# Kernel optimization log

Hardware: AMD Instinct MI355X
Metric: run time of the kernel (lower is better)

Reference implementation:

```python
import jax, jax.numpy as jnp
import numpy as np

MAX_Z = 54  # atomic numbers up to iodine (53)
_mv = np.full(MAX_Z, 4.0, np.float32)
for z, v in {6: 4, 7: 3, 8: 2, 16: 6, 9: 1, 17: 1, 35: 1, 53: 1, 15: 5, 1: 1}.items():
    _mv[z] = v
_vdw = np.full(MAX_Z, 1.6, np.float32)  # default_radius = 1.6
for z, r in {1: 1.2, 6: 1.7, 7: 1.55, 8: 1.52, 9: 1.47, 15: 1.8, 16: 1.8, 17: 1.75, 35: 1.85, 53: 1.98}.items():
    _vdw[z] = r
_bl = np.full((MAX_Z, MAX_Z), 1.5, np.float32)  # default_length = 1.5
for (a, b), L in {(6, 6): 1.54, (6, 7): 1.47, (6, 8): 1.43, (6, 16): 1.82, (6, 9): 1.35, (6, 17): 1.77, (6, 1): 1.09, (7, 7): 1.45, (7, 8): 1.40, (7, 1): 1.01, (8, 8): 1.48, (8, 1): 0.96, (16, 16): 2.05, (15, 8): 1.63}.items():
    _bl[a, b] = L
    _bl[b, a] = L  # symmetric == tuple(sorted(...)) lookup
MAX_VAL = jnp.asarray(_mv)
VDW = jnp.asarray(_vdw)
BOND = jnp.asarray(_bl)
BIG = 1e9  # stands in for torch's float('inf') diagonal mask


def _forward(pos, edge_index, atom_types):
    N = pos.shape[0]
    row, col = edge_index[0], edge_index[1]
    # --- valence violations: scatter-add out-degree per atom ---
    bond_counts = jnp.zeros((N,), pos.dtype).at[row].add(1.0)
    violation = jnp.maximum(bond_counts - MAX_VAL[atom_types], 0.0)  # >0 iff counts > max_val
    loss = jnp.sum(violation ** 2)
    # Sequential valence push. Original loops atoms in ascending order and each atom's
    # neighbors in edge-list order; a stable sort of edges by row reproduces exactly that
    # visitation order, so a scan over sorted edges matches the sequential semantics
    # (pos_new[i] updates feed later direction computations).
    order = jnp.argsort(row)  # jnp.argsort is stable
    rs, cs = row[order], col[order]

    def step(p, rc):
        r, c = rc
        v = violation[r]
        d = p[r] - p[c]
        dist = jnp.linalg.norm(d) + 1e-8
        return p.at[r].add(jnp.where(v > 0, d / dist * v * 1e-3, 0.0)), None

    pos_new, _ = jax.lax.scan(step, pos, (rs, cs))
    # --- bond-length correction (gather per edge, scatter back per atom) ---
    bond_vec = pos_new[row] - pos_new[col]                        # [E,3]
    cur_len = jnp.linalg.norm(bond_vec, axis=-1, keepdims=True)   # [E,1]
    tgt_len = BOND[atom_types[row], atom_types[col]][:, None]     # [E,1]
    loss = loss + jnp.mean(jnp.abs(cur_len - tgt_len) ** 2)
    ratio = jnp.clip(tgt_len / (cur_len + 1e-8), 0.98, 1.02)
    adj = (bond_vec * ratio - bond_vec) * 0.01
    pos_new = pos_new + jnp.zeros_like(pos).at[row].add(adj * 0.5).at[col].add(-adj * 0.5)
    # --- steric clash repulsion over all atom pairs (cdist) ---
    sq = jnp.sum(pos_new ** 2, axis=-1)
    d2 = sq[:, None] + sq[None, :] - 2.0 * (pos_new @ pos_new.T)  # [N,N]
    eye = jnp.eye(N, dtype=bool)
    dist = jnp.sqrt(jnp.maximum(jnp.where(eye, 1.0, d2), 1e-20))
    dist = jnp.where(eye, BIG, dist)  # diagonal masked to +inf in the original
    rad = VDW[atom_types]
    min_d = (rad[:, None] + rad[None, :]) * 0.8
    loss = loss + jnp.sum(jax.nn.relu(min_d - dist) ** 2) / 2.0
    # original loops unordered clash pairs i<j updating i and j symmetrically; the full
    # symmetric double sum below is mathematically identical and avoids an [N,N,3] tensor:
    mask = (dist < min_d) & (dist > 1e-8)
    coeff = jnp.where(mask, (min_d - dist) * 0.005 * 0.5 / dist, 0.0)  # [N,N]
    steric = coeff.sum(axis=1)[:, None] * pos_new - coeff @ pos_new    # sum_j c_ij (p_i - p_j)
    return pos_new + steric, loss * 0.1


def setup_inputs() -> dict:
    key = jax.random.key(0)
    k1, k2, k3, k4 = jax.random.split(key, 4)
    N, E = 8192, 32768
    pos = jax.random.normal(k1, (N, 3), jnp.float32) * 6.0  # coords in an ~Angstrom-scale blob
    elements = jnp.array([1, 6, 7, 8, 9, 15, 16, 17], jnp.int32)  # H C N O F P S Cl
    atom_types = elements[jax.random.randint(k2, (N,), 0, 8)]
    edge_index = jnp.stack([jax.random.randint(k3, (E,), 0, N),
                            jax.random.randint(k4, (E,), 0, N)]).astype(jnp.int32)
    return {"pos": pos, "edge_index": edge_index, "atom_types": atom_types}


def reference(pos, edge_index, atom_types):
    return _forward(pos, edge_index, atom_types)
```

## Files before the change

### kernel.cpp

```cpp
#include <hip/hip_runtime.h>
#include <math.h>

#define NA 8192
#define NE 32768
#define NT 256

#define WS_DEG      0
#define WS_LOSS     (WS_DEG + NA)
#define WS_DD       (WS_LOSS + 4)
#define WS_ZERO_END (WS_DD + 3*NA)
#define WS_PART     ((WS_ZERO_END + 3) & ~3)

__device__ __forceinline__ float maxval_of(int z) {
    switch (z) {
        case 1: return 1.f; case 6: return 4.f; case 7: return 3.f; case 8: return 2.f;
        case 9: return 1.f; case 15: return 5.f; case 16: return 6.f; case 17: return 1.f;
        case 35: return 1.f; case 53: return 1.f; default: return 4.f;
    }
}
__device__ __forceinline__ float vdw_of(int z) {
    switch (z) {
        case 1: return 1.2f; case 6: return 1.7f; case 7: return 1.55f; case 8: return 1.52f;
        case 9: return 1.47f; case 15: return 1.8f; case 16: return 1.8f; case 17: return 1.75f;
        case 35: return 1.85f; case 53: return 1.98f; default: return 1.6f;
    }
}
__device__ __forceinline__ float bond_of(int a, int b) {
    int lo = a < b ? a : b, hi = a < b ? b : a;
    switch (lo * 64 + hi) {
        case 6*64+6:   return 1.54f;
        case 6*64+7:   return 1.47f;
        case 6*64+8:   return 1.43f;
        case 6*64+16:  return 1.82f;
        case 6*64+9:   return 1.35f;
        case 6*64+17:  return 1.77f;
        case 1*64+6:   return 1.09f;
        case 7*64+7:   return 1.45f;
        case 7*64+8:   return 1.40f;
        case 1*64+7:   return 1.01f;
        case 8*64+8:   return 1.48f;
        case 1*64+8:   return 0.96f;
        case 16*64+16: return 2.05f;
        case 8*64+15:  return 1.63f;
        default:       return 1.5f;
    }
}
__device__ __forceinline__ float viol_of(int d, int z) {
    return fmaxf((float)d - maxval_of(z), 0.f);
}

__device__ __forceinline__ float wave_reduce_sum(float x) {
    #pragma unroll
    for (int off = 32; off > 0; off >>= 1) x += __shfl_down(x, off);
    return x;
}

__global__ void k_deg(const int* __restrict__ row, int* __restrict__ deg) {
    int e = blockIdx.x * NT + threadIdx.x;
    if (e < NE) atomicAdd(&deg[row[e]], 1);
}

__global__ void k_edge(const int* __restrict__ row, const int* __restrict__ col,
                       const int* __restrict__ types, const int* __restrict__ deg,
                       const float* __restrict__ pos, float* __restrict__ dD,
                       float* __restrict__ lossAcc) {
    int e = blockIdx.x * NT + threadIdx.x;
    float l1 = 0.f, l0 = 0.f;
    if (e < NE) {
        int r = row[e], c = col[e];
        float bx = pos[3*r]   - pos[3*c];
        float by = pos[3*r+1] - pos[3*c+1];
        float bz = pos[3*r+2] - pos[3*c+2];
        float cur = sqrtf(bx*bx + by*by + bz*bz);
        float tgt = bond_of(types[r], types[c]);
        float diff = cur - tgt;
        l1 = diff * diff;
        float ratio = tgt / (cur + 1e-8f);
        ratio = fminf(fmaxf(ratio, 0.98f), 1.02f);
        float s = (ratio - 1.f) * 0.01f * 0.5f;
        float v = viol_of(deg[r], types[r]);
        float sc = (v > 0.f) ? (v * 1e-3f / (cur + 1e-8f)) : 0.f;
        float rs = s + sc;
        atomicAdd(&dD[3*r],   bx * rs);
        atomicAdd(&dD[3*r+1], by * rs);
        atomicAdd(&dD[3*r+2], bz * rs);
        atomicAdd(&dD[3*c],   -bx * s);
        atomicAdd(&dD[3*c+1], -by * s);
        atomicAdd(&dD[3*c+2], -bz * s);
    }
    if (e < NA) {
        float v = viol_of(deg[e], types[e]);
        l0 = v * v;
    }
    float p1 = wave_reduce_sum(l1);
    float p0 = wave_reduce_sum(l0);
    if ((threadIdx.x & 63) == 0) {
        if (p1 != 0.f) atomicAdd(&lossAcc[1], p1);
        if (p0 != 0.f) atomicAdd(&lossAcc[0], p0);
    }
}

__device__ __forceinline__ void steric_pair(const float4 p, const float4 q,
                                            float& sx, float& sy, float& sz,
                                            float& ll) {
    float dx = p.x - q.x, dy = p.y - q.y, dz = p.z - q.z;
    float d2 = fmaf(dx, dx, fmaf(dy, dy, dz * dz));
    float md = p.w + q.w;
    float rinv = rsqrtf(fmaxf(d2, 1e-12f));
    float dist = d2 * rinv;
    float t1 = fmaxf(md - dist, 0.f);
    float t1c = (d2 > 1e-12f) ? t1 : 0.f;
    ll = fmaf(t1c, t1c, ll);
    float co = t1c * rinv;
    sx = fmaf(co, dx, sx);
    sy = fmaf(co, dy, sy);
    sz = fmaf(co, dz, sz);
}

template<int JSPLIT>
__global__ void __launch_bounds__(NT)
k_steric(const float* __restrict__ pos, const float* __restrict__ dD,
         const int* __restrict__ types, float4* __restrict__ partial,
         float* __restrict__ lossAcc) {
    constexpr int JCHUNK = NA / JSPLIT;
    constexpr int NIB    = NA / (NT * 2);
    __shared__ float4 sm[JCHUNK];
    const int t = threadIdx.x;
    const int b = blockIdx.x;
    const int yb = b / NIB;
    const int ib = b % NIB;
    if (t < JCHUNK) {
        int j = yb * JCHUNK + t;
        sm[t] = make_float4(pos[3*j]   + dD[3*j],
                            pos[3*j+1] + dD[3*j+1],
                            pos[3*j+2] + dD[3*j+2],
                            vdw_of(types[j]) * 0.8f);
    }
    const int i0 = ib * (NT * 2) + t;
    const int i1 = i0 + NT;
    float4 p0 = make_float4(pos[3*i0] + dD[3*i0], pos[3*i0+1] + dD[3*i0+1],
                            pos[3*i0+2] + dD[3*i0+2], vdw_of(types[i0]) * 0.8f);
    float4 p1 = make_float4(pos[3*i1] + dD[3*i1], pos[3*i1+1] + dD[3*i1+1],
                            pos[3*i1+2] + dD[3*i1+2], vdw_of(types[i1]) * 0.8f);
    __syncthreads();
    float sx0 = 0.f, sy0 = 0.f, sz0 = 0.f;
    float sx1 = 0.f, sy1 = 0.f, sz1 = 0.f;
    float ll = 0.f;
    #pragma unroll 8
    for (int jj = 0; jj < JCHUNK; jj++) {
        float4 q = sm[jj];
        steric_pair(p0, q, sx0, sy0, sz0, ll);
        steric_pair(p1, q, sx1, sy1, sz1, ll);
    }
    partial[yb * NA + i0] = make_float4(sx0, sy0, sz0, 0.f);
    partial[yb * NA + i1] = make_float4(sx1, sy1, sz1, 0.f);
    float part = wave_reduce_sum(ll);
    if ((t & 63) == 0 && part != 0.f) atomicAdd(&lossAcc[2], part);
}

template<int JSPLIT>
__global__ void k_reduce(const float* __restrict__ pos, const float* __restrict__ dD,
                         const float4* __restrict__ partial,
                         const float* __restrict__ lossAcc, float* __restrict__ out) {
    int a = blockIdx.x * NT + threadIdx.x;
    float sx = 0.f, sy = 0.f, sz = 0.f;
    #pragma unroll 8
    for (int y = 0; y < JSPLIT; y++) {
        float4 u = partial[y * NA + a];
        sx += u.x; sy += u.y; sz += u.z;
    }
    float px = pos[3*a]   + dD[3*a];
    float py = pos[3*a+1] + dD[3*a+1];
    float pz = pos[3*a+2] + dD[3*a+2];
    out[3*a]   = fmaf(sx, 0.0025f, px);
    out[3*a+1] = fmaf(sy, 0.0025f, py);
    out[3*a+2] = fmaf(sz, 0.0025f, pz);
    if (a == 0) {
        float loss = lossAcc[0] + lossAcc[1] * (1.f / NE) + lossAcc[2] * 0.5f;
        out[3*NA] = loss * 0.1f;
    }
}

extern "C" void kernel_launch(void* const* d_in, const int* in_sizes, int n_in,
                              void* d_out, int out_size, void* d_ws, size_t ws_size,
                              hipStream_t stream) {
    (void)in_sizes; (void)n_in; (void)out_size;
    const float* pos   = (const float*)d_in[0];
    const int*   eidx  = (const int*)d_in[1];
    const int*   types = (const int*)d_in[2];
    const int* row = eidx;
    const int* col = eidx + NE;

    int*   ws_i = (int*)d_ws;
    float* ws_f = (float*)d_ws;
    int*    deg     = ws_i + WS_DEG;
    float*  lossAcc = ws_f + WS_LOSS;
    float*  dD      = ws_f + WS_DD;
    float4* partial = (float4*)(ws_f + WS_PART);
    float*  out     = (float*)d_out;

    hipMemsetAsync(d_ws, 0, (size_t)WS_ZERO_END * 4, stream);
    k_deg   <<<NE/NT, NT, 0, stream>>>(row, deg);
    k_edge  <<<NE/NT, NT, 0, stream>>>(row, col, types, deg, pos, dD, lossAcc);

    const size_t need64 = (size_t)WS_PART * 4 + (size_t)64 * NA * sizeof(float4);
    constexpr int NIB = NA / (NT * 2);
    if (ws_size == 0 || ws_size >= need64) {
        k_steric<64><<<64 * NIB, NT, 0, stream>>>(pos, dD, types, partial, lossAcc);
        k_reduce<64><<<NA/NT, NT, 0, stream>>>(pos, dD, partial, lossAcc, out);
    } else {
        k_steric<32><<<32 * NIB, NT, 0, stream>>>(pos, dD, types, partial, lossAcc);
        k_reduce<32><<<NA/NT, NT, 0, stream>>>(pos, dD, partial, lossAcc, out);
    }
}
```

Baseline: 151.1 us.

## Simplify steric pair math, fix j-split at 32, fold zeroing into degree kernel

Rewrites the steric pair computation to derive the coefficient directly from md*rsqrt(d2)-1 and the loss from co^2*d2, removing a clamp, a multiply and a select per pair. Fixes the j-split at 32 with 256-entry shared chunks, batches shared-memory loads by 8, and sets launch bounds for two blocks per CU. Zeroing of loss and displacement buffers moves from the memset into the degree kernel, shrinking the memset. Fewer blocks may reduce parallelism but halves the partial-sum reduction work.

After: 140.4 us. -7.1%, faster.

```diff
diff --git a/kernel.cpp b/kernel.cpp
--- a/kernel.cpp
+++ b/kernel.cpp
@@ -4,6 +4,9 @@
 #define NA 8192
 #define NE 32768
 #define NT 256
+#define JSPLIT 32
+#define JCHUNK (NA / JSPLIT)
+#define NIB 16
 
 #define WS_DEG      0
 #define WS_LOSS     (WS_DEG + NA)
@@ -55,8 +58,10 @@
     return x;
 }
 
-__global__ void k_deg(const int* __restrict__ row, int* __restrict__ deg) {
+__global__ void k_deg(const int* __restrict__ row, int* __restrict__ deg,
+                      float* __restrict__ zbase ) {
     int e = blockIdx.x * NT + threadIdx.x;
+    if (e < 3 * NA + 4) zbase[e] = 0.f;
     if (e < NE) atomicAdd(&deg[row[e]], 1);
 }
 
@@ -105,39 +110,32 @@
                                             float& ll) {
     float dx = p.x - q.x, dy = p.y - q.y, dz = p.z - q.z;
     float d2 = fmaf(dx, dx, fmaf(dy, dy, dz * dz));
+    float rinv = rsqrtf(d2);
     float md = p.w + q.w;
-    float rinv = rsqrtf(fmaxf(d2, 1e-12f));
-    float dist = d2 * rinv;
-    float t1 = fmaxf(md - dist, 0.f);
-    float t1c = (d2 > 1e-12f) ? t1 : 0.f;
-    ll = fmaf(t1c, t1c, ll);
-    float co = t1c * rinv;
+    float co = fmaxf(fmaf(md, rinv, -1.f), 0.f);
+    co = (d2 > 1e-12f) ? co : 0.f;
+    ll = fmaf(co * co, d2, ll);
     sx = fmaf(co, dx, sx);
     sy = fmaf(co, dy, sy);
     sz = fmaf(co, dz, sz);
 }
 
-template<int JSPLIT>
-__global__ void __launch_bounds__(NT)
+__global__ void __launch_bounds__(NT, 2)
 k_steric(const float* __restrict__ pos, const float* __restrict__ dD,
          const int* __restrict__ types, float4* __restrict__ partial,
          float* __restrict__ lossAcc) {
-    constexpr int JCHUNK = NA / JSPLIT;
-    constexpr int NIB    = NA / (NT * 2);
     __shared__ float4 sm[JCHUNK];
     const int t = threadIdx.x;
     const int b = blockIdx.x;
-    const int yb = b / NIB;
-    const int ib = b % NIB;
-    if (t < JCHUNK) {
-        int j = yb * JCHUNK + t;
-        sm[t] = make_float4(pos[3*j]   + dD[3*j],
-                            pos[3*j+1] + dD[3*j+1],
-                            pos[3*j+2] + dD[3*j+2],
-                            vdw_of(types[j]) * 0.8f);
-    }
-    const int i0 = ib * (NT * 2) + t;
-    const int i1 = i0 + NT;
+    const int yb = b >> 4;
+    const int ib = b & 15;
+    int j = yb * JCHUNK + t;
+    sm[t] = make_float4(pos[3*j]   + dD[3*j],
+                        pos[3*j+1] + dD[3*j+1],
+                        pos[3*j+2] + dD[3*j+2],
+                        vdw_of(types[j]) * 0.8f);
+    const int i0 = ib * 512 + t;
+    const int i1 = i0 + 256;
     float4 p0 = make_float4(pos[3*i0] + dD[3*i0], pos[3*i0+1] + dD[3*i0+1],
                             pos[3*i0+2] + dD[3*i0+2], vdw_of(types[i0]) * 0.8f);
     float4 p1 = make_float4(pos[3*i1] + dD[3*i1], pos[3*i1+1] + dD[3*i1+1],
@@ -146,11 +144,15 @@
     float sx0 = 0.f, sy0 = 0.f, sz0 = 0.f;
     float sx1 = 0.f, sy1 = 0.f, sz1 = 0.f;
     float ll = 0.f;
-    #pragma unroll 8
-    for (int jj = 0; jj < JCHUNK; jj++) {
-        float4 q = sm[jj];
-        steric_pair(p0, q, sx0, sy0, sz0, ll);
-        steric_pair(p1, q, sx1, sy1, sz1, ll);
+    for (int jj = 0; jj < JCHUNK; jj += 8) {
+        float4 q[8];
+        #pragma unroll
+        for (int u = 0; u < 8; ++u) q[u] = sm[jj + u];
+        #pragma unroll
+        for (int u = 0; u < 8; ++u) {
+            steric_pair(p0, q[u], sx0, sy0, sz0, ll);
+            steric_pair(p1, q[u], sx1, sy1, sz1, ll);
+        }
     }
     partial[yb * NA + i0] = make_float4(sx0, sy0, sz0, 0.f);
     partial[yb * NA + i1] = make_float4(sx1, sy1, sz1, 0.f);
@@ -158,7 +160,6 @@
     if ((t & 63) == 0 && part != 0.f) atomicAdd(&lossAcc[2], part);
 }
 
-template<int JSPLIT>
 __global__ void k_reduce(const float* __restrict__ pos, const float* __restrict__ dD,
                          const float4* __restrict__ partial,
                          const float* __restrict__ lossAcc, float* __restrict__ out) {
@@ -184,7 +185,7 @@
 extern "C" void kernel_launch(void* const* d_in, const int* in_sizes, int n_in,
                               void* d_out, int out_size, void* d_ws, size_t ws_size,
                               hipStream_t stream) {
-    (void)in_sizes; (void)n_in; (void)out_size;
+    (void)in_sizes; (void)n_in; (void)out_size; (void)ws_size;
     const float* pos   = (const float*)d_in[0];
     const int*   eidx  = (const int*)d_in[1];
     const int*   types = (const int*)d_in[2];
@@ -199,17 +200,9 @@
     float4* partial = (float4*)(ws_f + WS_PART);
     float*  out     = (float*)d_out;
 
-    hipMemsetAsync(d_ws, 0, (size_t)WS_ZERO_END * 4, stream);
-    k_deg   <<<NE/NT, NT, 0, stream>>>(row, deg);
+    hipMemsetAsync(deg, 0, (size_t)NA * 4, stream);
+    k_deg   <<<NE/NT, NT, 0, stream>>>(row, deg, ws_f + WS_LOSS);
     k_edge  <<<NE/NT, NT, 0, stream>>>(row, col, types, deg, pos, dD, lossAcc);
-
-    const size_t need64 = (size_t)WS_PART * 4 + (size_t)64 * NA * sizeof(float4);
-    constexpr int NIB = NA / (NT * 2);
-    if (ws_size == 0 || ws_size >= need64) {
-        k_steric<64><<<64 * NIB, NT, 0, stream>>>(pos, dD, types, partial, lossAcc);
-        k_reduce<64><<<NA/NT, NT, 0, stream>>>(pos, dD, partial, lossAcc, out);
-    } else {
-        k_steric<32><<<32 * NIB, NT, 0, stream>>>(pos, dD, types, partial, lossAcc);
-        k_reduce<32><<<NA/NT, NT, 0, stream>>>(pos, dD, partial, lossAcc, out);
-    }
-}
+    k_steric<<<JSPLIT*NIB, NT, 0, stream>>>(pos, dD, types, partial, lossAcc);
+    k_reduce<<<NA/NT, NT, 0, stream>>>(pos, dD, partial, lossAcc, out);
+}
```
